# Optimization experiments

Hardware: AMD Instinct MI355X
Metric: run time of the kernel (lower is better)

## Reference

```python
import jax, jax.numpy as jnp
import numpy as np

N_HEAD = 16


def setup_inputs() -> dict:
    key = jax.random.key(0)
    ks = jax.random.split(key, 9)
    b, s, d = 4, 2048, 1024
    scale = 1.0 / np.sqrt(d)
    return {
        "x": jax.random.normal(ks[0], (b, s, d), dtype=jnp.float32),
        "Wq": jax.random.normal(ks[1], (d, d), dtype=jnp.float32) * scale,
        "bq": jax.random.normal(ks[2], (d,), dtype=jnp.float32) * 0.01,
        "Wk": jax.random.normal(ks[3], (d, d), dtype=jnp.float32) * scale,
        "bk": jax.random.normal(ks[4], (d,), dtype=jnp.float32) * 0.01,
        "Wv": jax.random.normal(ks[5], (d, d), dtype=jnp.float32) * scale,
        "bv": jax.random.normal(ks[6], (d,), dtype=jnp.float32) * 0.01,
        "Wo": jax.random.normal(ks[7], (d, d), dtype=jnp.float32) * scale,
        "bo": jax.random.normal(ks[8], (d,), dtype=jnp.float32) * 0.01,
        "mask": 1,
    }


def reference(x, Wq, bq, Wk, bk, Wv, bv, Wo, bo, mask):
    b, s, d = x.shape
    h = N_HEAD
    dh = d // h
    # projections -> [b, h, s, dh]
    def proj(W, bias):
        return (x @ W + bias).reshape(b, s, h, dh).transpose(0, 2, 1, 3)

    Q = proj(Wq, bq)
    K = proj(Wk, bk)
    V = proj(Wv, bv)

    # full S x S scores (module materializes them explicitly)
    scores = jnp.einsum('bhqd,bhkd->bhqk', Q, K)
    if mask:
        causal = jnp.triu(jnp.ones((s, s), dtype=bool), k=1)
        scores = jnp.where(causal, -jnp.inf, scores)
    scores = scores / jnp.sqrt(jnp.asarray(dh, dtype=scores.dtype))
    attn = jax.nn.softmax(scores, axis=-1)
    out = jnp.einsum('bhqk,bhkd->bhqd', attn, V)  # [b, h, s, dh]
    out = out.transpose(0, 2, 1, 3).reshape(b, s, d)
    return out @ Wo + bo
```

## Files before the change

kernel.cpp:

```cpp
#include <hip/hip_runtime.h>

typedef unsigned short u16;
typedef unsigned int u32;
typedef __bf16 bf16x4 __attribute__((ext_vector_type(4)));
typedef __bf16 bf16x8 __attribute__((ext_vector_type(8)));
typedef float f32x4 __attribute__((ext_vector_type(4)));
typedef float f32x16 __attribute__((ext_vector_type(16)));

#define BATCH 4
#define SLEN 2048
#define DMODEL 1024
#define NHEAD 16
#define DHEAD 64
#define MROWS (BATCH * SLEN)

__device__ __forceinline__ u16 f32_to_bf16(float f) {
  u32 u = __float_as_uint(f);
  u32 r = (u + 0x7FFFu + ((u >> 16) & 1u)) >> 16;
  return (u16)r;
}
__device__ __forceinline__ u32 pack_bf16x2(float a, float b) {
  return (u32)f32_to_bf16(a) | ((u32)f32_to_bf16(b) << 16);
}

__device__ __forceinline__ u32 pack_trunc(float lo, float hi) {
#if __has_builtin(__builtin_amdgcn_perm)
  return __builtin_amdgcn_perm(__float_as_uint(hi), __float_as_uint(lo), 0x07060302u);
#else
  return (__float_as_uint(hi) & 0xFFFF0000u) | (__float_as_uint(lo) >> 16);
#endif
}
__device__ __forceinline__ u32 pack_round(float lo, float hi) {
  u32 ul = __float_as_uint(lo) + 0x8000u;
  u32 uh = __float_as_uint(hi) + 0x8000u;
#if __has_builtin(__builtin_amdgcn_perm)
  return __builtin_amdgcn_perm(uh, ul, 0x07060302u);
#else
  return (uh & 0xFFFF0000u) | (ul >> 16);
#endif
}

#if __has_builtin(__builtin_amdgcn_exp2f)
#define EXP2(x) __builtin_amdgcn_exp2f(x)
#else
#define EXP2(x) exp2f(x)
#endif

typedef const __attribute__((address_space(1))) void* gas_cv;
typedef __attribute__((address_space(3))) void* las_v;
__device__ __forceinline__ void async16(const u16* g, u16* l) {
  __builtin_amdgcn_global_load_lds((gas_cv)g, (las_v)l, 16, 0, 0);
}


__global__ void convert_x_kernel(const float* __restrict__ x, u16* __restrict__ xb) {
  size_t i = ((size_t)blockIdx.x * 256 + threadIdx.x) * 8;
  float4 v0 = *(const float4*)(x + i);
  float4 v1 = *(const float4*)(x + i + 4);
  uint4 o;
  o.x = pack_bf16x2(v0.x, v0.y);
  o.y = pack_bf16x2(v0.z, v0.w);
  o.z = pack_bf16x2(v1.x, v1.y);
  o.w = pack_bf16x2(v1.z, v1.w);
  *(uint4*)(xb + i) = o;
}

__global__ void transpose_w_kernel(const float* __restrict__ Wq, const float* __restrict__ Wk,
                                   const float* __restrict__ Wv, const float* __restrict__ Wo,
                                   u16* __restrict__ wqkvt, u16* __restrict__ wot) {
  __shared__ float tile[32][33];
  int z = blockIdx.z;
  const float* src = (z == 0) ? Wq : (z == 1) ? Wk : (z == 2) ? Wv : Wo;
  u16* dst = (z < 3) ? (wqkvt + (size_t)z * DMODEL * DMODEL) : wot;
  int c0 = blockIdx.x * 32, r0 = blockIdx.y * 32;
  int tx = threadIdx.x & 31, ty = threadIdx.x >> 5;
#pragma unroll
  for (int i = 0; i < 4; ++i)
    tile[ty + 8 * i][tx] = src[(size_t)(r0 + ty + 8 * i) * DMODEL + c0 + tx];
  __syncthreads();
#pragma unroll
  for (int i = 0; i < 4; ++i)
    dst[(size_t)(c0 + ty + 8 * i) * DMODEL + r0 + tx] = f32_to_bf16(tile[tx][ty + 8 * i]);
}

__global__ void concat_bias_kernel(const float* __restrict__ bq, const float* __restrict__ bk,
                                   const float* __restrict__ bv, float* __restrict__ bqkv) {
  int i = blockIdx.x * 256 + threadIdx.x;
  float v = (i < 1024) ? bq[i] : (i < 2048) ? bk[i - 1024] : bv[i - 2048];
  bqkv[i] = v;
}

template <int OUT_BF16, int FUSE_V>
__global__ __launch_bounds__(256) void gemm_bt_kernel(const u16* __restrict__ A,
                                                      const u16* __restrict__ Bt,
                                                      const float* __restrict__ bias,
                                                      void* __restrict__ Cout,
                                                      u16* __restrict__ vtout,
                                                      int M, int N, int K) {
  __shared__ u16 sA[128 * 32];
  __shared__ u16 sB[128 * 32];
  const int tid = threadIdx.x;
  const int wv = tid >> 6, lane = tid & 63;
  const int wr = wv >> 1, wc = wv & 1;
  const int col = lane & 15, quad = lane >> 4;
  const int m0 = blockIdx.x * 128;
  const int n0 = blockIdx.y * 128;

  f32x4 acc[4][4] = {};

  const int lr = tid >> 2;
  const int ls = tid & 3;
  const size_t a_base = (size_t)(m0 + lr) * K + ls * 8;
  const size_t b_base = (size_t)(n0 + lr) * K + ls * 8;
  u16* ldsA0 = sA + ((tid >> 6) << 9);
  u16* ldsA1 = ldsA0 + 2048;
  u16* ldsB0 = sB + ((tid >> 6) << 9);
  u16* ldsB1 = ldsB0 + 2048;

  for (int k0 = 0; k0 < K; k0 += 32) {
    async16(A + a_base + k0, ldsA0);
    async16(A + a_base + (size_t)64 * K + k0, ldsA1);
    async16(Bt + b_base + k0, ldsB0);
    async16(Bt + b_base + (size_t)64 * K + k0, ldsB1);
    __syncthreads();
    bf16x8 af[4], bfr[4];
#pragma unroll
    for (int i = 0; i < 4; ++i)
      af[i] = *(const bf16x8*)(sA + (wr * 64 + i * 16 + col) * 32 + quad * 8);
#pragma unroll
    for (int j = 0; j < 4; ++j)
      bfr[j] = *(const bf16x8*)(sB + (wc * 64 + j * 16 + col) * 32 + quad * 8);
#pragma unroll
    for (int i = 0; i < 4; ++i)
#pragma unroll
      for (int j = 0; j < 4; ++j)
        acc[i][j] = __builtin_amdgcn_mfma_f32_16x16x32_bf16(af[i], bfr[j], acc[i][j], 0, 0, 0);
    __syncthreads();
  }

#pragma unroll
  for (int i = 0; i < 4; ++i) {
#pragma unroll
    for (int j = 0; j < 4; ++j) {
      int n = n0 + wc * 64 + j * 16 + col;
      float bia = bias[n];
      if (FUSE_V && n >= 2 * DMODEL) {
        const int hh = (n - 2 * DMODEL) >> 6, dh = n & 63;
        const int mb = m0 + wr * 64 + i * 16 + quad * 4;
        const int bb = mb >> 11, s0 = mb & 2047;
        uint2 pk;
        pk.x = pack_bf16x2(acc[i][j][0] + bia, acc[i][j][1] + bia);
        pk.y = pack_bf16x2(acc[i][j][2] + bia, acc[i][j][3] + bia);
        *(uint2*)(vtout + ((size_t)((bb * 16 + hh) * 64 + dh)) * SLEN + s0) = pk;
      } else {
        const int cstride = FUSE_V ? (2 * DMODEL) : N;
#pragma unroll
        for (int r = 0; r < 4; ++r) {
          int m = m0 + wr * 64 + i * 16 + quad * 4 + r;
          float v = acc[i][j][r] + bia;
          if (OUT_BF16)
            ((u16*)Cout)[(size_t)m * cstride + n] = f32_to_bf16(v);
          else
            ((float*)Cout)[(size_t)m * cstride + n] = v;
        }
      }
    }
  }
}

__global__ __launch_bounds__(256, 2) void attn_kernel(const u16* __restrict__ qk,
                                                      const u16* __restrict__ vt,
                                                      u16* __restrict__ out) {
  const int lid = blockIdx.y * 8 + blockIdx.x;
  const int xcd = lid & 7;
  const int local = lid >> 3;
  const int bh = xcd * 8 + (local & 7);
  const int bx = local >> 3;
  const int b = bh >> 4, h = bh & 15;
  const int tid = threadIdx.x;
  const int wv = tid >> 6, lane = tid & 63;
  const int c = lane & 31, hi = lane >> 5;
  const int sfirst = bx * 4 + wv;

  __shared__ u16 sK[2][64 * 64];
  __shared__ u16 sV[2][64 * 64];

  const u16* kbase = qk + ((size_t)(b * SLEN)) * (2 * DMODEL) + DMODEL + h * DHEAD;
  const u16* vbase = vt + ((size_t)bh * DHEAD) * SLEN;
  const float scl2 = 0.125f * 1.44269504088896f;

  const int lrow = lane >> 3;
  const int sga = (lane & 7) ^ lrow;
  const int r0a = wv * 16, r0b = wv * 16 + 8;
  const int cs = c & 7;

  for (int half = 0; half < 2; ++half) {
    const int s2 = half ? (63 - sfirst) : sfirst;
    const int qbase = s2 * 32;
    const int nt_own = s2 / 2 + 1;
    const int nt = half ? (32 - 2 * bx) : (2 * bx + 2);

    const u16* qrow =
        qk + ((size_t)(b * SLEN + qbase + c)) * (2 * DMODEL) + h * DHEAD + hi * 8;
    bf16x8 aQ[4];
#pragma unroll
    for (int ks = 0; ks < 4; ++ks) aQ[ks] = *(const bf16x8*)(qrow + ks * 16);

    f32x16 accO[2] = {};
    float m2 = -1e30f, l_i = 0.0f;

    async16(kbase + (size_t)(r0a + lrow) * (2 * DMODEL) + sga * 8, sK[0] + r0a * 64);
    async16(kbase + (size_t)(r0b + lrow) * (2 * DMODEL) + sga * 8, sK[0] + r0b * 64);
    async16(vbase + (size_t)(r0a + lrow) * SLEN + sga * 8, sV[0] + r0a * 64);
    async16(vbase + (size_t)(r0b + lrow) * SLEN + sga * 8, sV[0] + r0b * 64);

    for (int t = 0; t < nt; ++t) {
      const int kv0 = t * 64;
      const int cur = t & 1, nxt = cur ^ 1;

      if (t + 1 < nt) {
        const int kvn = kv0 + 64;
        async16(kbase + (size_t)(kvn + r0a + lrow) * (2 * DMODEL) + sga * 8, sK[nxt] + r0a * 64);
        async16(kbase + (size_t)(kvn + r0b + lrow) * (2 * DMODEL) + sga * 8, sK[nxt] + r0b * 64);
        async16(vbase + (size_t)(r0a + lrow) * SLEN + kvn + sga * 8, sV[nxt] + r0a * 64);
        async16(vbase + (size_t)(r0b + lrow) * SLEN + kvn + sga * 8, sV[nxt] + r0b * 64);
        asm volatile("s_waitcnt vmcnt(4)");
      } else {
        asm volatile("s_waitcnt vmcnt(0)");
      }
      __builtin_amdgcn_sched_barrier(0);
      __builtin_amdgcn_s_barrier();
      __builtin_amdgcn_sched_barrier(0);

      if (t < nt_own) {
        const u16* sKc = sK[cur];
        const u16* sVc = sV[cur];
        bf16x8 bK[2][4], bV[2][4];
#pragma unroll
        for (int m = 0; m < 2; ++m) {
          const int rb = (m * 32 + c) * 64;
#pragma unroll
          for (int ks = 0; ks < 4; ++ks) {
            bK[m][ks] = *(const bf16x8*)(sKc + rb + (((ks * 2 + hi) ^ cs) << 3));
            bf16x4 vlo = *(const bf16x4*)(sVc + rb + (((ks * 2) ^ cs) << 3) + 4 * hi);
            bf16x4 vhi = *(const bf16x4*)(sVc + rb + (((ks * 2 + 1) ^ cs) << 3) + 4 * hi);
            bV[m][ks] = __builtin_shufflevector(vlo, vhi, 0, 1, 2, 3, 4, 5, 6, 7);
          }
        }

        f32x16 accST[2] = {};
        __builtin_amdgcn_s_setprio(1);
#pragma unroll
        for (int ks = 0; ks < 4; ++ks)
#pragma unroll
          for (int m = 0; m < 2; ++m)
            accST[m] = __builtin_amdgcn_mfma_f32_32x32x16_bf16(bK[m][ks], aQ[ks],
                                                               accST[m], 0, 0, 0);
        __builtin_amdgcn_s_setprio(0);

        if (t == nt_own - 1) {
          const int q = qbase + c;
          const int kvh = kv0 + 4 * hi;
#pragma unroll
          for (int m = 0; m < 2; ++m)
#pragma unroll
            for (int r = 0; r < 16; ++r) {
              int kv = kvh + m * 32 + ((r & 3) + 8 * (r >> 2));
              if (kv > q) accST[m][r] = -1e30f;
            }
        }

        float h0 = fmaxf(fmaxf(accST[0][0], accST[0][1]), fmaxf(accST[0][2], accST[0][3]));
        float h1 = fmaxf(fmaxf(accST[0][4], accST[0][5]), fmaxf(accST[0][6], accST[0][7]));
        float h2 = fmaxf(fmaxf(accST[0][8], accST[0][9]), fmaxf(accST[0][10], accST[0][11]));
        float h3 = fmaxf(fmaxf(accST[0][12], accST[0][13]), fmaxf(accST[0][14], accST[0][15]));
        float h4 = fmaxf(fmaxf(accST[1][0], accST[1][1]), fmaxf(accST[1][2], accST[1][3]));
        float h5 = fmaxf(fmaxf(accST[1][4], accST[1][5]), fmaxf(accST[1][6], accST[1][7]));
        float h6 = fmaxf(fmaxf(accST[1][8], accST[1][9]), fmaxf(accST[1][10], accST[1][11]));
        float h7 = fmaxf(fmaxf(accST[1][12], accST[1][13]), fmaxf(accST[1][14], accST[1][15]));
        float rmax = fmaxf(fmaxf(fmaxf(h0, h1), fmaxf(h2, h3)),
                           fmaxf(fmaxf(h4, h5), fmaxf(h6, h7)));
        rmax = fmaxf(rmax, __shfl_xor(rmax, 32));
        float rmaxs = rmax * scl2;
        const bool noresc = __all(rmaxs <= m2);
        float mnew = noresc ? m2 : fmaxf(m2, rmaxs);
        float alpha = noresc ? 1.0f : EXP2(m2 - mnew);
        m2 = mnew;

        float s0 = 0.f, s1 = 0.f, s2s = 0.f, s3 = 0.f;
#pragma unroll
        for (int m = 0; m < 2; ++m) {
#pragma unroll
          for (int r = 0; r < 16; r += 4) {
            float p0 = EXP2(__builtin_fmaf(accST[m][r + 0], scl2, -mnew));
            float p1 = EXP2(__builtin_fmaf(accST[m][r + 1], scl2, -mnew));
            float p2 = EXP2(__builtin_fmaf(accST[m][r + 2], scl2, -mnew));
            float p3 = EXP2(__builtin_fmaf(accST[m][r + 3], scl2, -mnew));
            accST[m][r + 0] = p0;
            accST[m][r + 1] = p1;
            accST[m][r + 2] = p2;
            accST[m][r + 3] = p3;
            s0 += p0;
            s1 += p1;
            s2s += p2;
            s3 += p3;
          }
        }
        float sacc = (s0 + s1) + (s2s + s3);
        sacc += __shfl_xor(sacc, 32);
        if (noresc) {
          l_i += sacc;
        } else {
          l_i = l_i * alpha + sacc;
#pragma unroll
          for (int m = 0; m < 2; ++m)
#pragma unroll
            for (int r = 0; r < 16; ++r) accO[m][r] *= alpha;
        }

        bf16x8 aP[4];
#pragma unroll
        for (int m = 0; m < 2; ++m)
#pragma unroll
          for (int s = 0; s < 2; ++s) {
            union {
              uint4 u;
              bf16x8 v;
            } cvt;
            cvt.u.x = pack_trunc(accST[m][8 * s + 0], accST[m][8 * s + 1]);
            cvt.u.y = pack_trunc(accST[m][8 * s + 2], accST[m][8 * s + 3]);
            cvt.u.z = pack_trunc(accST[m][8 * s + 4], accST[m][8 * s + 5]);
            cvt.u.w = pack_trunc(accST[m][8 * s + 6], accST[m][8 * s + 7]);
            aP[m * 2 + s] = cvt.v;
          }

        __builtin_amdgcn_s_setprio(1);
#pragma unroll
        for (int ks = 0; ks < 4; ++ks)
#pragma unroll
          for (int m = 0; m < 2; ++m)
            accO[m] = __builtin_amdgcn_mfma_f32_32x32x16_bf16(bV[m][ks], aP[ks],
                                                              accO[m], 0, 0, 0);
        __builtin_amdgcn_s_setprio(0);
      }

      __builtin_amdgcn_sched_barrier(0);
      __builtin_amdgcn_s_barrier();
      __builtin_amdgcn_sched_barrier(0);
    }

    {
      float rl = 1.0f / l_i;
      size_t rowoff =
          ((size_t)(b * SLEN + qbase + c)) * DMODEL + h * DHEAD + 4 * hi;
#pragma unroll
      for (int m = 0; m < 2; ++m)
#pragma unroll
        for (int j = 0; j < 4; ++j) {
          uint2 pk;
          pk.x = pack_round(accO[m][4 * j + 0] * rl, accO[m][4 * j + 1] * rl);
          pk.y = pack_round(accO[m][4 * j + 2] * rl, accO[m][4 * j + 3] * rl);
          *(uint2*)(out + rowoff + m * 32 + 8 * j) = pk;
        }
    }
  }
}


extern "C" void kernel_launch(void* const* d_in, const int* in_sizes, int n_in,
                              void* d_out, int out_size, void* d_ws, size_t ws_size,
                              hipStream_t stream) {
  const float* x = (const float*)d_in[0];
  const float* Wq = (const float*)d_in[1];
  const float* bq = (const float*)d_in[2];
  const float* Wk = (const float*)d_in[3];
  const float* bk = (const float*)d_in[4];
  const float* Wv = (const float*)d_in[5];
  const float* bv = (const float*)d_in[6];
  const float* Wo = (const float*)d_in[7];
  const float* bo = (const float*)d_in[8];

  char* ws = (char*)d_ws;
  u16* xb = (u16*)ws;
  u16* wqkvt = (u16*)(ws + ((size_t)16 << 20));
  u16* wot = (u16*)(ws + ((size_t)22 << 20));
  u16* qk = (u16*)(ws + ((size_t)24 << 20));
  u16* vtp = (u16*)(ws + ((size_t)56 << 20));
  u16* attnO = (u16*)(ws + ((size_t)72 << 20));
  float* bqkv = (float*)(ws + ((size_t)88 << 20));

  convert_x_kernel<<<4096, 256, 0, stream>>>(x, xb);
  transpose_w_kernel<<<dim3(32, 32, 4), 256, 0, stream>>>(Wq, Wk, Wv, Wo, wqkvt, wot);
  concat_bias_kernel<<<12, 256, 0, stream>>>(bq, bk, bv, bqkv);
  gemm_bt_kernel<1, 1><<<dim3(64, 24), 256, 0, stream>>>(xb, wqkvt, bqkv, (void*)qk, vtp,
                                                         MROWS, 3 * DMODEL, DMODEL);
  attn_kernel<<<dim3(8, BATCH * NHEAD), 256, 0, stream>>>(qk, vtp, attnO);
  gemm_bt_kernel<0, 0><<<dim3(64, 8), 256, 0, stream>>>(attnO, wot, bo, d_out, nullptr,
                                                        MROWS, DMODEL, DMODEL);
}
```

Before: 277.0 us.

## Double-buffer LDS tiles in projection GEMM to overlap global loads with MFMA

The projection GEMM now keeps two LDS buffers for the A and B tiles and issues the async global-to-LDS loads for the next K step before computing on the current one. Explicit vmcnt waits and raw s_barriers with sched_barriers replace __syncthreads, so the next tile's loads can remain outstanding during compute. The aim is to hide global memory latency in the QKV and output projections. It doubles LDS use per block, which may lower occupancy, and correctness relies on the hand-written waitcnt counts.

New measurement: 266.4 us. -3.8%, faster.

```diff
diff --git a/kernel.cpp b/kernel.cpp
--- a/kernel.cpp
+++ b/kernel.cpp
@@ -97,8 +97,8 @@
                                                       void* __restrict__ Cout,
                                                       u16* __restrict__ vtout,
                                                       int M, int N, int K) {
-  __shared__ u16 sA[128 * 32];
-  __shared__ u16 sB[128 * 32];
+  __shared__ u16 sA[2][128 * 32];
+  __shared__ u16 sB[2][128 * 32];
   const int tid = threadIdx.x;
   const int wv = tid >> 6, lane = tid & 63;
   const int wr = wv >> 1, wc = wv & 1;
@@ -112,30 +112,47 @@
   const int ls = tid & 3;
   const size_t a_base = (size_t)(m0 + lr) * K + ls * 8;
   const size_t b_base = (size_t)(n0 + lr) * K + ls * 8;
-  u16* ldsA0 = sA + ((tid >> 6) << 9);
-  u16* ldsA1 = ldsA0 + 2048;
-  u16* ldsB0 = sB + ((tid >> 6) << 9);
-  u16* ldsB1 = ldsB0 + 2048;
-
-  for (int k0 = 0; k0 < K; k0 += 32) {
-    async16(A + a_base + k0, ldsA0);
-    async16(A + a_base + (size_t)64 * K + k0, ldsA1);
-    async16(Bt + b_base + k0, ldsB0);
-    async16(Bt + b_base + (size_t)64 * K + k0, ldsB1);
-    __syncthreads();
+  const int wvo = (tid >> 6) << 9;
+
+  async16(A + a_base, sA[0] + wvo);
+  async16(A + a_base + (size_t)64 * K, sA[0] + wvo + 2048);
+  async16(Bt + b_base, sB[0] + wvo);
+  async16(Bt + b_base + (size_t)64 * K, sB[0] + wvo + 2048);
+
+  const int nit = K >> 5;
+  for (int it = 0; it < nit; ++it) {
+    const int cur = it & 1, nxt = cur ^ 1;
+
+    if (it + 1 < nit) {
+      const int k0 = (it + 1) << 5;
+      async16(A + a_base + k0, sA[nxt] + wvo);
+      async16(A + a_base + (size_t)64 * K + k0, sA[nxt] + wvo + 2048);
+      async16(Bt + b_base + k0, sB[nxt] + wvo);
+      async16(Bt + b_base + (size_t)64 * K + k0, sB[nxt] + wvo + 2048);
+      asm volatile("s_waitcnt vmcnt(4)");
+    } else {
+      asm volatile("s_waitcnt vmcnt(0)");
+    }
+    __builtin_amdgcn_sched_barrier(0);
+    __builtin_amdgcn_s_barrier();
+    __builtin_amdgcn_sched_barrier(0);
+
     bf16x8 af[4], bfr[4];
 #pragma unroll
     for (int i = 0; i < 4; ++i)
-      af[i] = *(const bf16x8*)(sA + (wr * 64 + i * 16 + col) * 32 + quad * 8);
+      af[i] = *(const bf16x8*)(sA[cur] + (wr * 64 + i * 16 + col) * 32 + quad * 8);
 #pragma unroll
     for (int j = 0; j < 4; ++j)
-      bfr[j] = *(const bf16x8*)(sB + (wc * 64 + j * 16 + col) * 32 + quad * 8);
+      bfr[j] = *(const bf16x8*)(sB[cur] + (wc * 64 + j * 16 + col) * 32 + quad * 8);
 #pragma unroll
     for (int i = 0; i < 4; ++i)
 #pragma unroll
       for (int j = 0; j < 4; ++j)
         acc[i][j] = __builtin_amdgcn_mfma_f32_16x16x32_bf16(af[i], bfr[j], acc[i][j], 0, 0, 0);
-    __syncthreads();
+
+    __builtin_amdgcn_sched_barrier(0);
+    __builtin_amdgcn_s_barrier();
+    __builtin_amdgcn_sched_barrier(0);
   }
 
 #pragma unroll
```
